# Kernel tuning notes

Hardware: AMD Instinct MI355X
Metric: run time of the kernel (lower is better)

The kernel has to match this reference:

```python
import jax, jax.numpy as jnp
import numpy as np

STRIDE = 1
PAD = 3  # kernel_size // 2 = 7 // 2


def setup_inputs() -> dict:
    key = jax.random.key(0)
    k1, k2, k3 = jax.random.split(key, 3)
    B, Cin, T = 32, 128, 4096
    K, Cout, ks = 4, 256, 7
    x = jax.random.normal(k1, (B, Cin, T), dtype=jnp.float32)
    weight = jax.random.normal(k2, (K, Cout, Cin, ks), dtype=jnp.float32) * 0.01
    bias = jnp.zeros((K, Cout), dtype=jnp.float32)
    rw = jax.random.normal(k3, (K, Cin), dtype=jnp.float32) * 0.05
    rb = jnp.zeros((K,), dtype=jnp.float32)
    return {"x": x, "weight": weight, "bias": bias, "rw": rw, "rb": rb}


def reference(x, weight, bias, rw, rb):
    # x: [B, Cin, T]; weight: [K, Cout, Cin, ks]; bias: [K, Cout]
    K, Cout, Cin, ks = weight.shape
    B = x.shape[0]
    # routing: adaptive avg pool over T -> Linear -> softmax
    pooled = jnp.mean(x, axis=-1)                      # [B, Cin]
    alpha = jax.nn.softmax(pooled @ rw.T + rb, axis=-1)  # [B, K]
    # all K conv branches in one conv by folding K into out-channels
    w_all = weight.reshape(K * Cout, Cin, ks)
    y = jax.lax.conv_general_dilated(
        x, w_all, window_strides=(STRIDE,), padding=[(PAD, PAD)],
        dimension_numbers=("NCH", "OIH", "NCH"))      # [B, K*Cout, T']
    Tp = y.shape[-1]
    y = y.reshape(B, K, Cout, Tp) + bias[None, :, :, None]
    # softmax-routed weighted sum over the K branches
    out = jnp.einsum("bk,bkct->bct", alpha, y)         # [B, Cout, T']
    return out
```

## Files before the change

### kernel.cpp

```cpp
#include <hip/hip_runtime.h>
#include <stdint.h>


#define TP 4102

#define XT_OFF     0u
#define WEFF_OFF   33603584u
#define WT_OFF     48283648u
#define POOLED_OFF 51953664u
#define ALPHA_OFF  51970048u
#define BIAS_OFF   51970560u

typedef short short8 __attribute__((ext_vector_type(8)));
typedef float f32x4 __attribute__((ext_vector_type(4)));

__device__ __forceinline__ unsigned short f2bf(float f) {
  unsigned int u = __builtin_bit_cast(unsigned int, f);
  u += 0x7fffu + ((u >> 16) & 1u);
  return (unsigned short)(u >> 16);
}

__global__ __launch_bounds__(256) void k_transpose_pool(
    const float* __restrict__ x, unsigned short* __restrict__ xt,
    float* __restrict__ pooled) {
  __shared__ __align__(16) unsigned short xs[128 * 136];
  __shared__ float pbuf[128 * 33];
  int blk = blockIdx.x;
  int b = blk >> 5, tc = blk & 31;
  int t0 = tc << 7;
  int tid = threadIdx.x;
  int lane32 = tid & 31, grp8 = tid >> 5;

  #pragma unroll
  for (int i = 0; i < 16; ++i) {
    int ci = i * 8 + grp8;
    const float4 v = *(const float4*)(x + (size_t)(b * 128 + ci) * 4096 + t0 + lane32 * 4);
    unsigned short h0 = f2bf(v.x), h1 = f2bf(v.y), h2 = f2bf(v.z), h3 = f2bf(v.w);
    uint2 pk;
    pk.x = (unsigned)h0 | ((unsigned)h1 << 16);
    pk.y = (unsigned)h2 | ((unsigned)h3 << 16);
    *(uint2*)(&xs[ci * 136 + lane32 * 4]) = pk;
    pbuf[ci * 33 + lane32] = v.x + v.y + v.z + v.w;
  }
  __syncthreads();
  if (tid < 128) {
    float s = 0.f;
    #pragma unroll
    for (int l = 0; l < 32; ++l) s += pbuf[tid * 33 + l];
    atomicAdd(&pooled[b * 128 + tid], s);
  }
  #pragma unroll
  for (int it = 0; it < 8; ++it) {
    int idx = it * 256 + tid;
    int tr = idx & 127, g = idx >> 7;
    unsigned short h[8];
    #pragma unroll
    for (int u = 0; u < 8; ++u) h[u] = xs[(g * 8 + u) * 136 + tr];
    uint4 o;
    o.x = (unsigned)h[0] | ((unsigned)h[1] << 16);
    o.y = (unsigned)h[2] | ((unsigned)h[3] << 16);
    o.z = (unsigned)h[4] | ((unsigned)h[5] << 16);
    o.w = (unsigned)h[6] | ((unsigned)h[7] << 16);
    *(uint4*)(xt + ((size_t)(b * 16 + g) * TP + 3 + t0 + tr) * 8) = o;
  }
  uint4 z; z.x = z.y = z.z = z.w = 0;
  if (tc == 0 && tid < 64) {
    int g = tid >> 2, pr = tid & 3;
    if (pr < 3) *(uint4*)(xt + ((size_t)(b * 16 + g) * TP + pr) * 8) = z;
  }
  if (tc == 31 && tid < 64) {
    int g = tid >> 2, pr = tid & 3;
    if (pr < 3) *(uint4*)(xt + ((size_t)(b * 16 + g) * TP + 4099 + pr) * 8) = z;
  }
}

__global__ __launch_bounds__(256) void k_wt(const float* __restrict__ w,
                                            float* __restrict__ wt) {
  int gid = blockIdx.x * 256 + threadIdx.x;
  int ci = gid & 127;
  int kc = gid >> 7;
  const float* src = w + (size_t)gid * 7;
  #pragma unroll
  for (int s = 0; s < 7; ++s)
    wt[((size_t)kc * 7 + s) * 128 + ci] = src[s];
}

__global__ __launch_bounds__(128) void k_alpha(
    const float* __restrict__ pooled, const float* __restrict__ rw,
    const float* __restrict__ rb, const float* __restrict__ bias,
    float* __restrict__ alpha, float* __restrict__ bias_eff) {
  __shared__ float red[4][128];
  __shared__ float al[4];
  int b = blockIdx.x, tid = threadIdx.x;
  float p = pooled[b * 128 + tid] * (1.0f / 4096.0f);
  #pragma unroll
  for (int k = 0; k < 4; ++k) red[k][tid] = p * rw[k * 128 + tid];
  __syncthreads();
  if (tid < 4) {
    float s = rb[tid];
    for (int j = 0; j < 128; ++j) s += red[tid][j];
    red[tid][0] = s;
  }
  __syncthreads();
  if (tid == 0) {
    float m = red[0][0];
    for (int k = 1; k < 4; ++k) m = fmaxf(m, red[k][0]);
    float e0 = __expf(red[0][0] - m), e1 = __expf(red[1][0] - m);
    float e2 = __expf(red[2][0] - m), e3 = __expf(red[3][0] - m);
    float inv = 1.0f / (e0 + e1 + e2 + e3);
    al[0] = e0 * inv; al[1] = e1 * inv; al[2] = e2 * inv; al[3] = e3 * inv;
    #pragma unroll
    for (int k = 0; k < 4; ++k) alpha[b * 4 + k] = al[k];
  }
  __syncthreads();
  #pragma unroll
  for (int cc = 0; cc < 2; ++cc) {
    int c = cc * 128 + tid;
    float s = 0.f;
    #pragma unroll
    for (int k = 0; k < 4; ++k) s += al[k] * bias[k * 256 + c];
    bias_eff[b * 256 + c] = s;
  }
}

__global__ __launch_bounds__(256) void k_fold(const float* __restrict__ wt,
                                              const float* __restrict__ alpha,
                                              unsigned short* __restrict__ weff) {
  int idx = blockIdx.x * 256 + threadIdx.x;
  int g = idx & 7;
  int c = (idx >> 3) & 127;
  int rest = idx >> 10;
  int chunk = rest % 14;
  int bcb = rest / 14;
  int cb = bcb & 1, b = bcb >> 1;
  int s = chunk >> 1, half = chunk & 1;
  int cout = cb * 128 + c;
  float a[4];
  #pragma unroll
  for (int k = 0; k < 4; ++k) a[k] = alpha[b * 4 + k];
  float acc8[8];
  #pragma unroll
  for (int j = 0; j < 8; ++j) acc8[j] = 0.f;
  #pragma unroll
  for (int k = 0; k < 4; ++k) {
    const float* src = wt + (((size_t)(k * 256 + cout) * 7 + s) * 128 + half * 64 + g * 8);
    #pragma unroll
    for (int j = 0; j < 8; ++j) acc8[j] += a[k] * src[j];
  }
  unsigned short h[8];
  #pragma unroll
  for (int j = 0; j < 8; ++j) h[j] = f2bf(acc8[j]);
  uint4 o;
  o.x = (unsigned)h[0] | ((unsigned)h[1] << 16);
  o.y = (unsigned)h[2] | ((unsigned)h[3] << 16);
  o.z = (unsigned)h[4] | ((unsigned)h[5] << 16);
  o.w = (unsigned)h[6] | ((unsigned)h[7] << 16);
  int kk = g >> 2, q = g & 3;
  int cblk = c >> 4, n16 = c & 15;
  int step = chunk * 2 + kk;
  size_t off8 = ((size_t)(bcb * 28 + step) * 8 + cblk) * 64 + q * 16 + n16;
  *(uint4*)(weff + off8 * 8) = o;
}

__global__ __launch_bounds__(256, 4) void k_conv(
    const unsigned short* __restrict__ xt, const unsigned short* __restrict__ weff,
    const float* __restrict__ bias_eff, float* __restrict__ out) {
  __shared__ __align__(16) unsigned short xs[16 * 136 * 8];
  int blk = blockIdx.x;
  int b = blk >> 6, cb = (blk >> 5) & 1, tb = blk & 31;
  int bcb = b * 2 + cb;
  int tid = threadIdx.x;
  int wave = tid >> 6, lane = tid & 63;
  int q = lane >> 4, n16 = lane & 15;
  int wm = wave & 1, wn = wave >> 1;
  int t00 = tb << 7;

  const unsigned short* xtb = xt + (size_t)b * 16 * TP * 8;
  #pragma unroll
  for (int it = 0; it < 8; ++it) {
    int idx = it * 256 + tid;
    int g = idx >> 7, row = idx & 127;
    uint4 v = *(const uint4*)(xtb + ((size_t)g * TP + t00 + row) * 8);
    *(uint4*)(&xs[(g * 136 + row) * 8]) = v;
  }
  if (tid < 128) {
    int g = tid >> 3, r8 = tid & 7;
    if (r8 < 6) {
      int row = 128 + r8;
      uint4 v = *(const uint4*)(xtb + ((size_t)g * TP + t00 + row) * 8);
      *(uint4*)(&xs[(g * 136 + row) * 8]) = v;
    }
  }
  __syncthreads();

  f32x4 acc[4][4];
  #pragma unroll
  for (int mi = 0; mi < 4; ++mi)
    #pragma unroll
    for (int ni = 0; ni < 4; ++ni)
      acc[mi][ni] = (f32x4){0.f, 0.f, 0.f, 0.f};

  const short8* wfrag = (const short8*)weff + (size_t)bcb * 14336 + (wm * 4) * 64 + lane;

  short8 av[4];
  #pragma unroll
  for (int mi = 0; mi < 4; ++mi) av[mi] = wfrag[mi * 64];

  #pragma unroll 2
  for (int step = 0; step < 28; ++step) {
    int s = step >> 2, half = (step >> 1) & 1, kk = step & 1;
    short8 avn[4];
    if (step < 27) {
      #pragma unroll
      for (int mi = 0; mi < 4; ++mi)
        avn[mi] = wfrag[(step + 1) * 512 + mi * 64];
    }
    short8 bv[4];
    #pragma unroll
    for (int ni = 0; ni < 4; ++ni) {
      int tt = wn * 64 + ni * 16 + n16;
      bv[ni] = *(const short8*)(&xs[((half * 8 + kk * 4 + q) * 136 + tt + s) * 8]);
    }
    #pragma unroll
    for (int mi = 0; mi < 4; ++mi)
      #pragma unroll
      for (int ni = 0; ni < 4; ++ni)
        acc[mi][ni] = __builtin_amdgcn_mfma_f32_16x16x32_bf16(
            av[mi], bv[ni], acc[mi][ni], 0, 0, 0);
    #pragma unroll
    for (int mi = 0; mi < 4; ++mi) av[mi] = avn[mi];
  }

  int crow0 = b * 256 + cb * 128;
  #pragma unroll
  for (int mi = 0; mi < 4; ++mi) {
    #pragma unroll
    for (int r = 0; r < 4; ++r) {
      int c = wm * 64 + mi * 16 + q * 4 + r;
      float bb = bias_eff[crow0 + c];
      float* orow = out + (size_t)(crow0 + c) * 4096 + t00;
      #pragma unroll
      for (int ni = 0; ni < 4; ++ni)
        orow[wn * 64 + ni * 16 + n16] = acc[mi][ni][r] + bb;
    }
  }
}

extern "C" void kernel_launch(void* const* d_in, const int* in_sizes, int n_in,
                              void* d_out, int out_size, void* d_ws, size_t ws_size,
                              hipStream_t stream) {
  const float* x    = (const float*)d_in[0];
  const float* w    = (const float*)d_in[1];
  const float* bias = (const float*)d_in[2];
  const float* rw   = (const float*)d_in[3];
  const float* rb   = (const float*)d_in[4];
  float* out = (float*)d_out;
  char* ws = (char*)d_ws;
  unsigned short* xt   = (unsigned short*)(ws + XT_OFF);
  unsigned short* weff = (unsigned short*)(ws + WEFF_OFF);
  float* wt            = (float*)(ws + WT_OFF);
  float* pooled        = (float*)(ws + POOLED_OFF);
  float* alpha         = (float*)(ws + ALPHA_OFF);
  float* bias_eff      = (float*)(ws + BIAS_OFF);

  hipMemsetAsync(pooled, 0, 32 * 128 * sizeof(float), stream);
  hipLaunchKernelGGL(k_transpose_pool, dim3(1024), dim3(256), 0, stream, x, xt, pooled);
  hipLaunchKernelGGL(k_wt,    dim3(512),  dim3(256), 0, stream, w, wt);
  hipLaunchKernelGGL(k_alpha, dim3(32),   dim3(128), 0, stream, pooled, rw, rb, bias, alpha, bias_eff);
  hipLaunchKernelGGL(k_fold,  dim3(3584), dim3(256), 0, stream, wt, alpha, weff);
  hipLaunchKernelGGL(k_conv,  dim3(2048), dim3(256), 0, stream, xt, weff, bias_eff, out);
}
```

Measured before the change: 255.4 us.

## Fuse weight transpose, routing and fold into one kernel; widen conv time tile

```diff
diff --git a/kernel.cpp b/kernel.cpp
--- a/kernel.cpp
+++ b/kernel.cpp
@@ -6,10 +6,8 @@
 
 #define XT_OFF     0u
 #define WEFF_OFF   33603584u
-#define WT_OFF     48283648u
-#define POOLED_OFF 51953664u
-#define ALPHA_OFF  51970048u
-#define BIAS_OFF   51970560u
+#define POOLED_OFF 48283648u
+#define BEFF_OFF   48300032u
 
 typedef short short8 __attribute__((ext_vector_type(8)));
 typedef float f32x4 __attribute__((ext_vector_type(4)));
@@ -74,130 +72,111 @@
   }
 }
 
-__global__ __launch_bounds__(256) void k_wt(const float* __restrict__ w,
-                                            float* __restrict__ wt) {
-  int gid = blockIdx.x * 256 + threadIdx.x;
-  int ci = gid & 127;
-  int kc = gid >> 7;
-  const float* src = w + (size_t)gid * 7;
-  #pragma unroll
-  for (int s = 0; s < 7; ++s)
-    wt[((size_t)kc * 7 + s) * 128 + ci] = src[s];
-}
-
-__global__ __launch_bounds__(128) void k_alpha(
-    const float* __restrict__ pooled, const float* __restrict__ rw,
-    const float* __restrict__ rb, const float* __restrict__ bias,
-    float* __restrict__ alpha, float* __restrict__ bias_eff) {
-  __shared__ float red[4][128];
-  __shared__ float al[4];
-  int b = blockIdx.x, tid = threadIdx.x;
-  float p = pooled[b * 128 + tid] * (1.0f / 4096.0f);
-  #pragma unroll
-  for (int k = 0; k < 4; ++k) red[k][tid] = p * rw[k * 128 + tid];
-  __syncthreads();
-  if (tid < 4) {
-    float s = rb[tid];
-    for (int j = 0; j < 128; ++j) s += red[tid][j];
-    red[tid][0] = s;
-  }
-  __syncthreads();
-  if (tid == 0) {
-    float m = red[0][0];
-    for (int k = 1; k < 4; ++k) m = fmaxf(m, red[k][0]);
-    float e0 = __expf(red[0][0] - m), e1 = __expf(red[1][0] - m);
-    float e2 = __expf(red[2][0] - m), e3 = __expf(red[3][0] - m);
+__global__ __launch_bounds__(256) void k_fold(
+    const float* __restrict__ w, const float* __restrict__ pooled,
+    const float* __restrict__ rw, const float* __restrict__ rb,
+    const float* __restrict__ bias, unsigned short* __restrict__ weff,
+    float* __restrict__ bias_eff) {
+  __shared__ float al[32][4];
+  int tid = threadIdx.x;
+  if (tid < 128) {
+    int b = tid >> 2, k = tid & 3;
+    const float* pp = pooled + b * 128;
+    const float* rwk = rw + k * 128;
+    float s = rb[k];
+    #pragma unroll 8
+    for (int j = 0; j < 128; ++j) s += pp[j] * (1.0f / 4096.0f) * rwk[j];
+    al[b][k] = s;
+  }
+  __syncthreads();
+  if (tid < 32) {
+    float l0 = al[tid][0], l1 = al[tid][1], l2 = al[tid][2], l3 = al[tid][3];
+    float m = fmaxf(fmaxf(l0, l1), fmaxf(l2, l3));
+    float e0 = __expf(l0 - m), e1 = __expf(l1 - m);
+    float e2 = __expf(l2 - m), e3 = __expf(l3 - m);
     float inv = 1.0f / (e0 + e1 + e2 + e3);
-    al[0] = e0 * inv; al[1] = e1 * inv; al[2] = e2 * inv; al[3] = e3 * inv;
-    #pragma unroll
-    for (int k = 0; k < 4; ++k) alpha[b * 4 + k] = al[k];
-  }
-  __syncthreads();
-  #pragma unroll
-  for (int cc = 0; cc < 2; ++cc) {
-    int c = cc * 128 + tid;
-    float s = 0.f;
-    #pragma unroll
-    for (int k = 0; k < 4; ++k) s += al[k] * bias[k * 256 + c];
-    bias_eff[b * 256 + c] = s;
-  }
-}
-
-__global__ __launch_bounds__(256) void k_fold(const float* __restrict__ wt,
-                                              const float* __restrict__ alpha,
-                                              unsigned short* __restrict__ weff) {
-  int idx = blockIdx.x * 256 + threadIdx.x;
-  int g = idx & 7;
-  int c = (idx >> 3) & 127;
-  int rest = idx >> 10;
-  int chunk = rest % 14;
-  int bcb = rest / 14;
-  int cb = bcb & 1, b = bcb >> 1;
-  int s = chunk >> 1, half = chunk & 1;
-  int cout = cb * 128 + c;
-  float a[4];
-  #pragma unroll
-  for (int k = 0; k < 4; ++k) a[k] = alpha[b * 4 + k];
-  float acc8[8];
-  #pragma unroll
-  for (int j = 0; j < 8; ++j) acc8[j] = 0.f;
+    al[tid][0] = e0 * inv; al[tid][1] = e1 * inv;
+    al[tid][2] = e2 * inv; al[tid][3] = e3 * inv;
+  }
+  __syncthreads();
+  if (blockIdx.x == 0) {
+    #pragma unroll
+    for (int b = 0; b < 32; ++b) {
+      float s = 0.f;
+      #pragma unroll
+      for (int k = 0; k < 4; ++k) s += al[b][k] * bias[k * 256 + tid];
+      bias_eff[b * 256 + tid] = s;
+    }
+  }
+  int gid = blockIdx.x * 256 + tid;
+  int cb = gid / 14336;
+  int r = gid - cb * 14336;
+  int step = r >> 9;
+  int cblk = (r >> 6) & 7;
+  int lpos = r & 63;
+  int q = lpos >> 4, n16 = lpos & 15;
+  int kk = step & 1, half = (step >> 1) & 1, s7 = step >> 2;
+  int cout = cb * 128 + cblk * 16 + n16;
+  int ci0 = half * 64 + (kk * 4 + q) * 8;
+  float wv[4][8];
   #pragma unroll
   for (int k = 0; k < 4; ++k) {
-    const float* src = wt + (((size_t)(k * 256 + cout) * 7 + s) * 128 + half * 64 + g * 8);
-    #pragma unroll
-    for (int j = 0; j < 8; ++j) acc8[j] += a[k] * src[j];
-  }
-  unsigned short h[8];
-  #pragma unroll
-  for (int j = 0; j < 8; ++j) h[j] = f2bf(acc8[j]);
-  uint4 o;
-  o.x = (unsigned)h[0] | ((unsigned)h[1] << 16);
-  o.y = (unsigned)h[2] | ((unsigned)h[3] << 16);
-  o.z = (unsigned)h[4] | ((unsigned)h[5] << 16);
-  o.w = (unsigned)h[6] | ((unsigned)h[7] << 16);
-  int kk = g >> 2, q = g & 3;
-  int cblk = c >> 4, n16 = c & 15;
-  int step = chunk * 2 + kk;
-  size_t off8 = ((size_t)(bcb * 28 + step) * 8 + cblk) * 64 + q * 16 + n16;
-  *(uint4*)(weff + off8 * 8) = o;
-}
-
-__global__ __launch_bounds__(256, 4) void k_conv(
+    const float* src = w + ((size_t)(k * 256 + cout) * 128 + ci0) * 7 + s7;
+    #pragma unroll
+    for (int j = 0; j < 8; ++j) wv[k][j] = src[j * 7];
+  }
+  unsigned short* dst =
+      weff + (((size_t)(cb * 28 + step) * 8 + cblk) * 64 + lpos) * 8;
+  #pragma unroll 4
+  for (int b = 0; b < 32; ++b) {
+    float a0 = al[b][0], a1 = al[b][1], a2 = al[b][2], a3 = al[b][3];
+    unsigned short h[8];
+    #pragma unroll
+    for (int j = 0; j < 8; ++j)
+      h[j] = f2bf(a0 * wv[0][j] + a1 * wv[1][j] + a2 * wv[2][j] + a3 * wv[3][j]);
+    uint4 o;
+    o.x = (unsigned)h[0] | ((unsigned)h[1] << 16);
+    o.y = (unsigned)h[2] | ((unsigned)h[3] << 16);
+    o.z = (unsigned)h[4] | ((unsigned)h[5] << 16);
+    o.w = (unsigned)h[6] | ((unsigned)h[7] << 16);
+    *(uint4*)(dst + (size_t)b * 229376) = o;
+  }
+}
+
+__global__ __launch_bounds__(256, 2) void k_conv(
     const unsigned short* __restrict__ xt, const unsigned short* __restrict__ weff,
     const float* __restrict__ bias_eff, float* __restrict__ out) {
-  __shared__ __align__(16) unsigned short xs[16 * 136 * 8];
+  __shared__ __align__(16) unsigned short xs[16 * 262 * 8];
   int blk = blockIdx.x;
-  int b = blk >> 6, cb = (blk >> 5) & 1, tb = blk & 31;
+  int b = blk >> 5, cb = (blk >> 4) & 1, tb = blk & 15;
   int bcb = b * 2 + cb;
   int tid = threadIdx.x;
   int wave = tid >> 6, lane = tid & 63;
   int q = lane >> 4, n16 = lane & 15;
   int wm = wave & 1, wn = wave >> 1;
-  int t00 = tb << 7;
+  int t00 = tb << 8;
 
   const unsigned short* xtb = xt + (size_t)b * 16 * TP * 8;
   #pragma unroll
-  for (int it = 0; it < 8; ++it) {
-    int idx = it * 256 + tid;
-    int g = idx >> 7, row = idx & 127;
-    uint4 v = *(const uint4*)(xtb + ((size_t)g * TP + t00 + row) * 8);
-    *(uint4*)(&xs[(g * 136 + row) * 8]) = v;
+  for (int g = 0; g < 16; ++g) {
+    *(uint4*)(&xs[((size_t)g * 262 + tid) * 8]) =
+        *(const uint4*)(xtb + ((size_t)g * TP + t00 + tid) * 8);
   }
   if (tid < 128) {
     int g = tid >> 3, r8 = tid & 7;
     if (r8 < 6) {
-      int row = 128 + r8;
-      uint4 v = *(const uint4*)(xtb + ((size_t)g * TP + t00 + row) * 8);
-      *(uint4*)(&xs[(g * 136 + row) * 8]) = v;
-    }
-  }
-  __syncthreads();
-
-  f32x4 acc[4][4];
+      int row = 256 + r8;
+      *(uint4*)(&xs[((size_t)g * 262 + row) * 8]) =
+          *(const uint4*)(xtb + ((size_t)g * TP + t00 + row) * 8);
+    }
+  }
+  __syncthreads();
+
+  f32x4 acc[4][8];
   #pragma unroll
   for (int mi = 0; mi < 4; ++mi)
     #pragma unroll
-    for (int ni = 0; ni < 4; ++ni)
+    for (int ni = 0; ni < 8; ++ni)
       acc[mi][ni] = (f32x4){0.f, 0.f, 0.f, 0.f};
 
   const short8* wfrag = (const short8*)weff + (size_t)bcb * 14336 + (wm * 4) * 64 + lane;
@@ -215,16 +194,17 @@
       for (int mi = 0; mi < 4; ++mi)
         avn[mi] = wfrag[(step + 1) * 512 + mi * 64];
     }
-    short8 bv[4];
-    #pragma unroll
-    for (int ni = 0; ni < 4; ++ni) {
-      int tt = wn * 64 + ni * 16 + n16;
-      bv[ni] = *(const short8*)(&xs[((half * 8 + kk * 4 + q) * 136 + tt + s) * 8]);
+    short8 bv[8];
+    int prow = (half * 8 + kk * 4 + q) * 262 + s;
+    #pragma unroll
+    for (int ni = 0; ni < 8; ++ni) {
+      int tt = wn * 128 + ni * 16 + n16;
+      bv[ni] = *(const short8*)(&xs[(size_t)(prow + tt) * 8]);
     }
     #pragma unroll
     for (int mi = 0; mi < 4; ++mi)
       #pragma unroll
-      for (int ni = 0; ni < 4; ++ni)
+      for (int ni = 0; ni < 8; ++ni)
         acc[mi][ni] = __builtin_amdgcn_mfma_f32_16x16x32_bf16(
             av[mi], bv[ni], acc[mi][ni], 0, 0, 0);
     #pragma unroll
@@ -240,8 +220,8 @@
       float bb = bias_eff[crow0 + c];
       float* orow = out + (size_t)(crow0 + c) * 4096 + t00;
       #pragma unroll
-      for (int ni = 0; ni < 4; ++ni)
-        orow[wn * 64 + ni * 16 + n16] = acc[mi][ni][r] + bb;
+      for (int ni = 0; ni < 8; ++ni)
+        orow[wn * 128 + ni * 16 + n16] = acc[mi][ni][r] + bb;
     }
   }
 }
@@ -258,15 +238,12 @@
   char* ws = (char*)d_ws;
   unsigned short* xt   = (unsigned short*)(ws + XT_OFF);
   unsigned short* weff = (unsigned short*)(ws + WEFF_OFF);
-  float* wt            = (float*)(ws + WT_OFF);
   float* pooled        = (float*)(ws + POOLED_OFF);
-  float* alpha         = (float*)(ws + ALPHA_OFF);
-  float* bias_eff      = (float*)(ws + BIAS_OFF);
+  float* bias_eff      = (float*)(ws + BEFF_OFF);
 
   hipMemsetAsync(pooled, 0, 32 * 128 * sizeof(float), stream);
   hipLaunchKernelGGL(k_transpose_pool, dim3(1024), dim3(256), 0, stream, x, xt, pooled);
-  hipLaunchKernelGGL(k_wt,    dim3(512),  dim3(256), 0, stream, w, wt);
-  hipLaunchKernelGGL(k_alpha, dim3(32),   dim3(128), 0, stream, pooled, rw, rb, bias, alpha, bias_eff);
-  hipLaunchKernelGGL(k_fold,  dim3(3584), dim3(256), 0, stream, wt, alpha, weff);
-  hipLaunchKernelGGL(k_conv,  dim3(2048), dim3(256), 0, stream, xt, weff, bias_eff, out);
-}
+  hipLaunchKernelGGL(k_fold, dim3(112), dim3(256), 0, stream,
+                     w, pooled, rw, rb, bias, weff, bias_eff);
+  hipLaunchKernelGGL(k_conv, dim3(1024), dim3(256), 0, stream, xt, weff, bias_eff, out);
+}
```

Result: faster. 249.6 us (-2.3%).
